# Kernel optimization log

Measured on AMD Instinct MI355X. Metric: run time of the kernel, lower is better.

Reference implementation:

```python
import jax, jax.numpy as jnp
import numpy as np

N, E = 100000, 1600000
IN, EDGE_DIM, HID, OUT, HEADS = 128, 16, 32, 32, 2


def _glorot(key, shape, scale=0.1):
    return jax.random.normal(key, shape, dtype=jnp.float32) * scale


def setup_inputs() -> dict:
    key = jax.random.key(0)
    ks = jax.random.split(key, 20)
    HC1 = HEADS * HID
    return {
        "x": jax.random.normal(ks[0], (N, IN), dtype=jnp.float32),
        "edge_index": jax.random.randint(ks[1], (2, E), 0, N, dtype=jnp.int32),
        "edge_attr": jax.random.normal(ks[2], (E, EDGE_DIM), dtype=jnp.float32),
        # layer 1 (heads=HEADS, concat=True)
        "W1l": _glorot(ks[3], (IN, HC1)), "b1l": jnp.zeros((HC1,), jnp.float32),
        "W1r": _glorot(ks[4], (IN, HC1)), "b1r": jnp.zeros((HC1,), jnp.float32),
        "W1e": _glorot(ks[5], (EDGE_DIM, HC1)),
        "att1": _glorot(ks[6], (HEADS, HID)),
        "bias1": jnp.zeros((HC1,), jnp.float32),
        # layer 2 (heads=1, concat=False)
        "W2l": _glorot(ks[7], (HC1, HID)), "b2l": jnp.zeros((HID,), jnp.float32),
        "W2r": _glorot(ks[8], (HC1, HID)), "b2r": jnp.zeros((HID,), jnp.float32),
        "W2e": _glorot(ks[9], (EDGE_DIM, HID)),
        "att2": _glorot(ks[10], (1, HID)),
        "bias2": jnp.zeros((HID,), jnp.float32),
        # final linear
        "Wlin": _glorot(ks[11], (HID, OUT)), "blin": jnp.zeros((OUT,), jnp.float32),
    }


def gatv2_layer(x, src, dst, edge_attr, Wl, bl, Wr, br, We, att, bias, H, C, concat):
    n = x.shape[0]
    xl = (x @ Wl + bl).reshape(n, H, C)   # source transform (lin_l)
    xr = (x @ Wr + br).reshape(n, H, C)   # target transform (lin_r)
    ea = (edge_attr @ We).reshape(-1, H, C)
    m = xl[src] + xr[dst] + ea                       # [E, H, C]
    e = jnp.sum(jax.nn.leaky_relu(m, 0.2) * att, axis=-1)  # [E, H]
    # segment softmax over incoming edges of each destination node
    emax = jax.ops.segment_max(e, dst, num_segments=n)
    emax = jnp.where(jnp.isfinite(emax), emax, 0.0)
    ee = jnp.exp(e - emax[dst])
    denom = jax.ops.segment_sum(ee, dst, num_segments=n)
    alpha = ee / (denom[dst] + 1e-16)                # [E, H]
    out = jax.ops.segment_sum(xl[src] * alpha[..., None], dst, num_segments=n)  # [N, H, C]
    out = out.reshape(n, H * C) if concat else out.mean(axis=1)
    return out + bias


def reference(x, edge_index, edge_attr, W1l, b1l, W1r, b1r, W1e, att1, bias1,
              W2l, b2l, W2r, b2r, W2e, att2, bias2, Wlin, blin):
    src, dst = edge_index[0], edge_index[1]
    h = jax.nn.elu(gatv2_layer(x, src, dst, edge_attr, W1l, b1l, W1r, b1r, W1e,
                               att1, bias1, HEADS, HID, True))
    h = jax.nn.elu(gatv2_layer(h, src, dst, edge_attr, W2l, b2l, W2r, b2r, W2e,
                               att2, bias2, 1, HID, False))
    return h @ Wlin + blin
```

## Files before the change

kernel.cpp:

```cpp
#include <hip/hip_runtime.h>
#include <hip/hip_fp16.h>
#include <cstdint>
#include <cstddef>


typedef _Float16 half8 __attribute__((ext_vector_type(8)));
typedef float f32x4 __attribute__((ext_vector_type(4)));

__global__ void hist_kernel(const int* __restrict__ dst, int* __restrict__ deg, int E) {
    int e = blockIdx.x * blockDim.x + threadIdx.x;
    if (e < E) atomicAdd(&deg[dst[e]], 1);
}

__global__ void scan_part(const int* __restrict__ deg, int* __restrict__ bsum, int n) {
    int tid = threadIdx.x;
    int base = blockIdx.x * 1024 + tid * 4;
    int s = 0;
#pragma unroll
    for (int j = 0; j < 4; ++j) {
        int i = base + j;
        if (i < n) s += deg[i];
    }
#pragma unroll
    for (int off = 1; off < 64; off <<= 1) s += __shfl_xor(s, off, 64);
    __shared__ int ws[4];
    if ((tid & 63) == 0) ws[tid >> 6] = s;
    __syncthreads();
    if (tid == 0) bsum[blockIdx.x] = ws[0] + ws[1] + ws[2] + ws[3];
}

__global__ void scan_mid(int* __restrict__ bsum, int* __restrict__ rowstart, int nb, int n) {
    int tid = threadIdx.x;
    int v = (tid < nb) ? bsum[tid] : 0;
    int incl = v;
#pragma unroll
    for (int off = 1; off < 64; off <<= 1) {
        int t = __shfl_up(incl, off, 64);
        if ((tid & 63) >= off) incl += t;
    }
    __shared__ int w0;
    if (tid == 63) w0 = incl;
    __syncthreads();
    if (tid >= 64) incl += w0;
    if (tid < nb) bsum[tid] = incl - v;
    if (tid == nb - 1) rowstart[n] = incl;
}

__global__ void scan_fin(const int* __restrict__ deg, const int* __restrict__ bsum,
                         int* __restrict__ rowstart, int n) {
    int tid = threadIdx.x;
    int lane = tid & 63, wid = tid >> 6;
    int base = blockIdx.x * 1024 + tid * 4;
    int v[4];
    int s = 0;
#pragma unroll
    for (int j = 0; j < 4; ++j) {
        int i = base + j;
        v[j] = (i < n) ? deg[i] : 0;
        s += v[j];
    }
    int incl = s;
#pragma unroll
    for (int off = 1; off < 64; off <<= 1) {
        int t = __shfl_up(incl, off, 64);
        if (lane >= off) incl += t;
    }
    __shared__ int ws[4];
    if (lane == 63) ws[wid] = incl;
    __syncthreads();
    int wofs = 0;
    for (int w2 = 0; w2 < wid; ++w2) wofs += ws[w2];
    int acc = bsum[blockIdx.x] + wofs + (incl - s);
#pragma unroll
    for (int j = 0; j < 4; ++j) {
        int i = base + j;
        if (i < n) rowstart[i] = acc;
        acc += v[j];
    }
}

__global__ void scatter_kernel(const int* __restrict__ src, const int* __restrict__ dst,
                               const float* __restrict__ eattr,
                               const int* __restrict__ rowstart, int* __restrict__ cursor,
                               int2* __restrict__ es, __half* __restrict__ eah, int E) {
    int e = blockIdx.x * blockDim.x + threadIdx.x;
    if (e < E) {
        int d = dst[e];
        int p = atomicAdd(&cursor[d], 1);
        es[rowstart[d] + p] = make_int2(e, src[e]);
        const float4* s4 = (const float4*)&eattr[(size_t)e * 16];
        float4 a = s4[0], b = s4[1], c = s4[2], f = s4[3];
        __half2 h[8];
        h[0] = __float22half2_rn(make_float2(a.x, a.y));
        h[1] = __float22half2_rn(make_float2(a.z, a.w));
        h[2] = __float22half2_rn(make_float2(b.x, b.y));
        h[3] = __float22half2_rn(make_float2(b.z, b.w));
        h[4] = __float22half2_rn(make_float2(c.x, c.y));
        h[5] = __float22half2_rn(make_float2(c.z, c.w));
        h[6] = __float22half2_rn(make_float2(f.x, f.y));
        h[7] = __float22half2_rn(make_float2(f.z, f.w));
        int4* o = (int4*)&eah[(size_t)e * 16];
        o[0] = *(int4*)&h[0];
        o[1] = *(int4*)&h[4];
    }
}

__global__ __launch_bounds__(1024) void dcount_block(const int* __restrict__ deg,
                                                     int* __restrict__ counts, int n) {
    __shared__ int h[256];
    int tid = threadIdx.x;
    if (tid < 256) h[tid] = 0;
    __syncthreads();
    int base = blockIdx.x * 4096 + tid;
#pragma unroll
    for (int j = 0; j < 4; ++j) {
        int i = base + j * 1024;
        if (i < n) {
            int b = deg[i];
            b = (b > 255) ? 255 : b;
            atomicAdd(&h[b], 1);
        }
    }
    __syncthreads();
    if (tid < 256) counts[blockIdx.x * 256 + tid] = h[tid];
}

__global__ void dbase_kernel(const int* __restrict__ counts, int* __restrict__ base, int nblk) {
    int b = threadIdx.x;
    int tot = 0;
    for (int k = 0; k < nblk; ++k) tot += counts[k * 256 + b];
    __shared__ int ws[4];
    int lane = b & 63, wid = b >> 6;
    int incl = tot;
#pragma unroll
    for (int off = 1; off < 64; off <<= 1) {
        int t = __shfl_up(incl, off, 64);
        if (lane >= off) incl += t;
    }
    if (lane == 63) ws[wid] = incl;
    __syncthreads();
    int wofs = 0;
    for (int w = 0; w < wid; ++w) wofs += ws[w];
    int acc = wofs + incl - tot;
    for (int k = 0; k < nblk; ++k) {
        base[k * 256 + b] = acc;
        acc += counts[k * 256 + b];
    }
}

__global__ __launch_bounds__(1024) void dscatter_block(const int* __restrict__ deg,
                                                       const int* __restrict__ base,
                                                       int* __restrict__ nodeperm, int n) {
    __shared__ int h[256];
    int tid = threadIdx.x;
    if (tid < 256) h[tid] = 0;
    __syncthreads();
    int bbase = blockIdx.x * 4096 + tid;
#pragma unroll
    for (int j = 0; j < 4; ++j) {
        int i = bbase + j * 1024;
        if (i < n) {
            int b = deg[i];
            b = (b > 255) ? 255 : b;
            int r = atomicAdd(&h[b], 1);
            nodeperm[base[blockIdx.x * 256 + b] + r] = i;
        }
    }
}

template <int K, int Mh>
__global__ void wprep_kernel(const float* __restrict__ Wl, const float* __restrict__ Wr,
                             __half* __restrict__ Wfrag) {
    constexpr int KS = K / 32;
    constexpr int BN = 2 * Mh;
    int i = blockIdx.x * blockDim.x + threadIdx.x;
    if (i >= K * BN) return;
    int j = i & 7;
    int lane = (i >> 3) & 63;
    int rest = i >> 9;
    int ks = rest % KS;
    int nt = rest / KS;
    int k = ks * 32 + ((lane >> 4) & 3) * 8 + j;
    int col = nt * 16 + (lane & 15);
    float v = (col < Mh) ? Wl[k * Mh + col] : Wr[k * Mh + (col - Mh)];
    Wfrag[i] = __float2half(v);
}

template <int K, int Mh, int BM>
__global__ __launch_bounds__(256) void gemm_mfma(
    const float* __restrict__ x, const __half* __restrict__ Wfrag,
    const float* __restrict__ bl, const float* __restrict__ br,
    __half* __restrict__ yl, __half* __restrict__ yr, int n) {
    constexpr int BN = 2 * Mh;
    constexpr int KS = K / 32;
    constexpr int NT = BN / 16;
    constexpr int RW = BM / 64;
    constexpr int LDP = K + 8;
    __shared__ __half xs[BM * LDP];
    int tid = threadIdx.x;
    int lane = tid & 63;
    int wave = tid >> 6;
    int node0 = blockIdx.x * BM;
    constexpr int ITER = (BM * K) / (256 * 4);
#pragma unroll
    for (int it = 0; it < ITER; ++it) {
        int base = (it * 256 + tid) * 4;
        int row = base / K, kk = base % K;
        float4 v = make_float4(0.f, 0.f, 0.f, 0.f);
        if (node0 + row < n) v = *(const float4*)&x[(size_t)(node0 + row) * K + kk];
        __half2* d = (__half2*)&xs[row * LDP + kk];
        d[0] = __float22half2_rn(make_float2(v.x, v.y));
        d[1] = __float22half2_rn(make_float2(v.z, v.w));
    }
    __syncthreads();
    f32x4 acc[RW][NT];
#pragma unroll
    for (int r = 0; r < RW; ++r)
#pragma unroll
        for (int t = 0; t < NT; ++t) {
            f32x4 z = {0.f, 0.f, 0.f, 0.f};
            acc[r][t] = z;
        }
    int r0 = lane & 15, kof = (lane >> 4) * 8;
#pragma unroll
    for (int ks = 0; ks < KS; ++ks) {
        half8 a[RW];
#pragma unroll
        for (int r = 0; r < RW; ++r) {
            int row = (wave * RW + r) * 16 + r0;
            a[r] = *reinterpret_cast<const half8*>(&xs[row * LDP + ks * 32 + kof]);
        }
#pragma unroll
        for (int t = 0; t < NT; ++t) {
            half8 b = *reinterpret_cast<const half8*>(&Wfrag[(((size_t)t * KS + ks) * 64 + lane) * 8]);
#pragma unroll
            for (int r = 0; r < RW; ++r)
                acc[r][t] = __builtin_amdgcn_mfma_f32_16x16x32_f16(a[r], b, acc[r][t], 0, 0, 0);
        }
    }
#pragma unroll
    for (int r = 0; r < RW; ++r) {
#pragma unroll
        for (int t = 0; t < NT; ++t) {
            int col = t * 16 + (lane & 15);
            float bv = (col < Mh) ? bl[col] : br[col - Mh];
#pragma unroll
            for (int q = 0; q < 4; ++q) {
                int node = node0 + (wave * RW + r) * 16 + (lane >> 4) * 4 + q;
                if (node < n) {
                    float v = acc[r][t][q] + bv;
                    if (col < Mh) yl[(size_t)node * Mh + col] = __float2half(v);
                    else          yr[(size_t)node * Mh + (col - Mh)] = __float2half(v);
                }
            }
        }
    }
}

template <int K, int M, int NPB>
__global__ void linear_kernel(const float* __restrict__ x, const float* __restrict__ W,
                              const float* __restrict__ b, float* __restrict__ y, int n) {
    __shared__ float sx[NPB * K];
    int tid = threadIdx.x;
    int node0 = blockIdx.x * NPB;
    for (int i = tid; i < NPB * K; i += NPB * M) {
        int nn = node0 + i / K;
        sx[i] = (nn < n) ? x[(size_t)nn * K + (i % K)] : 0.f;
    }
    __syncthreads();
    int ln = tid / M, m = tid % M;
    int node = node0 + ln;
    if (node >= n) return;
    float acc = b[m];
#pragma unroll
    for (int k = 0; k < K; ++k) acc = fmaf(sx[ln * K + k], W[k * M + m], acc);
    y[(size_t)node * M + m] = acc;
}

template <int H, int C>
__global__ __launch_bounds__(256) void fused_edge_agg(
    const int* __restrict__ rowstart, const int2* __restrict__ es,
    const __half* __restrict__ eah, const int* __restrict__ nodeperm,
    const float* __restrict__ We,
    const float* __restrict__ att,
    const __half* __restrict__ xl, const __half* __restrict__ xr,
    const float* __restrict__ bias, float* __restrict__ out, int n) {
    constexpr int HC = H * C;
    constexpr int LPN = HC / 2;
    constexpr int NPW = 64 / LPN;
    int gt = blockIdx.x * blockDim.x + threadIdx.x;
    int wave = gt >> 6;
    int lane = threadIdx.x & 63;
    int sub = lane / LPN;
    int j = lane % LPN;
    int ch0 = 2 * j;
    int slot = wave * NPW + sub;
    if (slot >= n) return;
    int node = nodeperm[slot];
    __half2 wh[16];
#pragma unroll
    for (int k = 0; k < 16; ++k) wh[k] = __float22half2_rn(*(const float2*)&We[k * HC + ch0]);
    float2 a2 = *(const float2*)&att[ch0];
    float2 xr2 = __half22float2(*(const __half2*)&xr[(size_t)node * HC + ch0]);
    int beg = rowstart[node], end = rowstart[node + 1];
    float denom = 0.f, acc0 = 0.f, acc1 = 0.f;

    auto gemv = [&](const float4& r0, const float4& r1, const __half2& xlh,
                    float& m0, float& m1, float2& xlf) {
        const __half2* h0 = (const __half2*)&r0;
        const __half2* h1 = (const __half2*)&r1;
        __half2 p0 = __hmul2(__low2half2(h0[0]), wh[0]);
        __half2 p1 = __hmul2(__high2half2(h0[0]), wh[1]);
        p0 = __hfma2(__low2half2(h0[1]), wh[2], p0);
        p1 = __hfma2(__high2half2(h0[1]), wh[3], p1);
        p0 = __hfma2(__low2half2(h0[2]), wh[4], p0);
        p1 = __hfma2(__high2half2(h0[2]), wh[5], p1);
        p0 = __hfma2(__low2half2(h0[3]), wh[6], p0);
        p1 = __hfma2(__high2half2(h0[3]), wh[7], p1);
        p0 = __hfma2(__low2half2(h1[0]), wh[8], p0);
        p1 = __hfma2(__high2half2(h1[0]), wh[9], p1);
        p0 = __hfma2(__low2half2(h1[1]), wh[10], p0);
        p1 = __hfma2(__high2half2(h1[1]), wh[11], p1);
        p0 = __hfma2(__low2half2(h1[2]), wh[12], p0);
        p1 = __hfma2(__high2half2(h1[2]), wh[13], p1);
        p0 = __hfma2(__low2half2(h1[3]), wh[14], p0);
        p1 = __hfma2(__high2half2(h1[3]), wh[15], p1);
        float2 mf = __half22float2(__hadd2(p0, p1));
        xlf = __half22float2(xlh);
        m0 = xlf.x + xr2.x + mf.x;
        m1 = xlf.y + xr2.y + mf.y;
    };
    auto logit = [&](float m0, float m1) -> float {
        m0 = (m0 > 0.f) ? m0 : 0.2f * m0;
        m1 = (m1 > 0.f) ? m1 : 0.2f * m1;
        float v = m0 * a2.x + m1 * a2.y;
#pragma unroll
        for (int msk = 1; msk < 16; msk <<= 1) v += __shfl_xor(v, msk, 64);
        return v;
    };

    int pp = beg;
    for (; pp + 2 <= end; pp += 2) {
        int2 ea = es[pp];
        int2 eb = es[pp + 1];
        const float4* qa = (const float4*)&eah[(size_t)ea.x * 16];
        const float4* qb = (const float4*)&eah[(size_t)eb.x * 16];
        float4 r0a = qa[0], r1a = qa[1];
        float4 r0b = qb[0], r1b = qb[1];
        __half2 xh0 = *(const __half2*)&xl[(size_t)ea.y * HC + ch0];
        __half2 xh1 = *(const __half2*)&xl[(size_t)eb.y * HC + ch0];
        float m0a, m1a, m0b, m1b;
        float2 xla, xlb;
        gemv(r0a, r1a, xh0, m0a, m1a, xla);
        gemv(r0b, r1b, xh1, m0b, m1b, xlb);
        float wa = __expf(logit(m0a, m1a));
        float wb = __expf(logit(m0b, m1b));
        denom += wa + wb;
        acc0 = fmaf(xla.x, wa, acc0);
        acc1 = fmaf(xla.y, wa, acc1);
        acc0 = fmaf(xlb.x, wb, acc0);
        acc1 = fmaf(xlb.y, wb, acc1);
    }
    if (pp < end) {
        int2 ea = es[pp];
        const float4* qa = (const float4*)&eah[(size_t)ea.x * 16];
        float4 r0a = qa[0], r1a = qa[1];
        __half2 xh0 = *(const __half2*)&xl[(size_t)ea.y * HC + ch0];
        float m0a, m1a;
        float2 xla;
        gemv(r0a, r1a, xh0, m0a, m1a, xla);
        float wa = __expf(logit(m0a, m1a));
        denom += wa;
        acc0 = fmaf(xla.x, wa, acc0);
        acc1 = fmaf(xla.y, wa, acc1);
    }
    float2 b2 = *(const float2*)&bias[ch0];
    float inv = 1.f / (denom + 1e-16f);
    float o0 = acc0 * inv + b2.x;
    float o1 = acc1 * inv + b2.y;
    o0 = (o0 > 0.f) ? o0 : __expf(o0) - 1.f;
    o1 = (o1 > 0.f) ? o1 : __expf(o1) - 1.f;
    *(float2*)&out[(size_t)node * HC + ch0] = make_float2(o0, o1);
}

extern "C" void kernel_launch(void* const* d_in, const int* in_sizes, int n_in,
                              void* d_out, int out_size, void* d_ws, size_t ws_size,
                              hipStream_t stream) {
    const float* x     = (const float*)d_in[0];
    const int*   eidx  = (const int*)d_in[1];
    const float* eattr = (const float*)d_in[2];
    const float* W1l   = (const float*)d_in[3];
    const float* b1l   = (const float*)d_in[4];
    const float* W1r   = (const float*)d_in[5];
    const float* b1r   = (const float*)d_in[6];
    const float* W1e   = (const float*)d_in[7];
    const float* att1  = (const float*)d_in[8];
    const float* bias1 = (const float*)d_in[9];
    const float* W2l   = (const float*)d_in[10];
    const float* b2l   = (const float*)d_in[11];
    const float* W2r   = (const float*)d_in[12];
    const float* b2r   = (const float*)d_in[13];
    const float* W2e   = (const float*)d_in[14];
    const float* att2  = (const float*)d_in[15];
    const float* bias2 = (const float*)d_in[16];
    const float* Wlin  = (const float*)d_in[17];
    const float* blin  = (const float*)d_in[18];

    const int N = in_sizes[0] / 128;
    const int E = in_sizes[1] / 2;
    const int* src = eidx;
    const int* dst = eidx + E;
    const int NBLK = (N + 4095) / 4096;

    char* p = (char*)d_ws;
    auto take = [&](size_t bytes) {
        char* r = p;
        p += (bytes + 255) & ~(size_t)255;
        return r;
    };
    int*    deg      = (int*)take((size_t)N * sizeof(int));
    int*    cursor   = (int*)take((size_t)N * sizeof(int));
    char*   zero_end = p;
    int*    rowstart = (int*)take((size_t)(N + 1) * sizeof(int));
    int*    bsum     = (int*)take(256 * sizeof(int));
    int*    counts   = (int*)take((size_t)(NBLK + 1) * 256 * sizeof(int));
    int*    dbase    = (int*)take((size_t)(NBLK + 1) * 256 * sizeof(int));
    int*    nodeperm = (int*)take((size_t)N * sizeof(int));
    int2*   es       = (int2*)take((size_t)E * sizeof(int2));
    __half* eah      = (__half*)take((size_t)E * 16 * sizeof(__half));
    __half* A        = (__half*)take((size_t)N * 64 * sizeof(__half));
    __half* B        = (__half*)take((size_t)N * 64 * sizeof(__half));
    float*  Cbuf     = (float*)take((size_t)N * 64 * sizeof(float));
    __half* Wf1      = (__half*)take((size_t)128 * 128 * sizeof(__half));
    __half* Wf2      = (__half*)take((size_t)64 * 64 * sizeof(__half));

    (void)hipMemsetAsync(deg, 0, (size_t)(zero_end - (char*)deg), stream);
    hist_kernel<<<(E + 255) / 256, 256, 0, stream>>>(dst, deg, E);
    {
        int nb = (N + 1023) / 1024;
        scan_part<<<nb, 256, 0, stream>>>(deg, bsum, N);
        scan_mid<<<1, 128, 0, stream>>>(bsum, rowstart, nb, N);
        scan_fin<<<nb, 256, 0, stream>>>(deg, bsum, rowstart, N);
    }
    scatter_kernel<<<(E + 255) / 256, 256, 0, stream>>>(src, dst, eattr, rowstart, cursor, es,
                                                        eah, E);
    dcount_block<<<NBLK, 1024, 0, stream>>>(deg, counts, N);
    dbase_kernel<<<1, 256, 0, stream>>>(counts, dbase, NBLK);
    dscatter_block<<<NBLK, 1024, 0, stream>>>(deg, dbase, nodeperm, N);
    wprep_kernel<128, 64><<<(128 * 128 + 255) / 256, 256, 0, stream>>>(W1l, W1r, Wf1);
    wprep_kernel<64, 32><<<(64 * 64 + 255) / 256, 256, 0, stream>>>(W2l, W2r, Wf2);

    gemm_mfma<128, 64, 64><<<(N + 63) / 64, 256, 0, stream>>>(x, Wf1, b1l, b1r, A, B, N);
    {
        long waves = (N + 1) / 2;
        fused_edge_agg<2, 32><<<(int)((waves * 64 + 255) / 256), 256, 0, stream>>>(
            rowstart, es, eah, nodeperm, W1e, att1, A, B, bias1, Cbuf, N);
    }

    gemm_mfma<64, 32, 128><<<(N + 127) / 128, 256, 0, stream>>>(Cbuf, Wf2, b2l, b2r, A, B, N);
    {
        long waves = (N + 3) / 4;
        fused_edge_agg<1, 32><<<(int)((waves * 64 + 255) / 256), 256, 0, stream>>>(
            rowstart, es, eah, nodeperm, W2e, att2, A, B, bias2, Cbuf, N);
    }

    linear_kernel<32, 32, 8><<<(N + 7) / 8, 256, 0, stream>>>(Cbuf, Wlin, blin, (float*)d_out, N);
}
```

Measured before the change: 421.2 us.

## Fuse setup kernels into one launch and materialize dst-sorted edge attributes

Merges the layer-1 GEMM, the edge scatter and the degree-count kernels into a single multi-role launch, and merges the two weight-prep kernels into one. The interleaved (eid,src) array is split into separate eid and src arrays. When workspace allows, layer-1 edge aggregation writes the edge attributes in destination-sorted order so layer 2 reads them contiguously instead of gathering by edge id. This trades an extra write of the edge-attribute buffer and more workspace for fewer launches and a coalesced read in layer 2.

```diff
diff --git a/kernel.cpp b/kernel.cpp
--- a/kernel.cpp
+++ b/kernel.cpp
@@ -79,15 +79,109 @@
     }
 }
 
-__global__ void scatter_kernel(const int* __restrict__ src, const int* __restrict__ dst,
-                               const float* __restrict__ eattr,
-                               const int* __restrict__ rowstart, int* __restrict__ cursor,
-                               int2* __restrict__ es, __half* __restrict__ eah, int E) {
-    int e = blockIdx.x * blockDim.x + threadIdx.x;
+template <int K, int Mh>
+__device__ void wprep_body(int i, const float* __restrict__ Wl, const float* __restrict__ Wr,
+                           __half* __restrict__ Wfrag) {
+    constexpr int KS = K / 32;
+    if (i >= K * 2 * Mh) return;
+    int j = i & 7;
+    int lane = (i >> 3) & 63;
+    int rest = i >> 9;
+    int ks = rest % KS;
+    int nt = rest / KS;
+    int k = ks * 32 + ((lane >> 4) & 3) * 8 + j;
+    int col = nt * 16 + (lane & 15);
+    float v = (col < Mh) ? Wl[k * Mh + col] : Wr[k * Mh + (col - Mh)];
+    Wfrag[i] = __float2half(v);
+}
+
+__global__ void wprep_both(const float* W1l, const float* W1r, __half* Wf1,
+                           const float* W2l, const float* W2r, __half* Wf2) {
+    int bid = blockIdx.x;
+    int tid = threadIdx.x;
+    if (bid < 64) wprep_body<128, 64>(bid * 256 + tid, W1l, W1r, Wf1);
+    else          wprep_body<64, 32>((bid - 64) * 256 + tid, W2l, W2r, Wf2);
+}
+
+template <int K, int Mh, int BM>
+__device__ void gemm_body(int bid, __half* xs, const float* __restrict__ x,
+                          const __half* __restrict__ Wfrag, const float* __restrict__ bl,
+                          const float* __restrict__ br, __half* __restrict__ yl,
+                          __half* __restrict__ yr, int n) {
+    constexpr int KS = K / 32;
+    constexpr int NT = (2 * Mh) / 16;
+    constexpr int RW = BM / 64;
+    constexpr int LDP = K + 8;
+    int tid = threadIdx.x;
+    int lane = tid & 63;
+    int wave = tid >> 6;
+    int node0 = bid * BM;
+    constexpr int ITER = (BM * K) / (256 * 4);
+#pragma unroll
+    for (int it = 0; it < ITER; ++it) {
+        int base = (it * 256 + tid) * 4;
+        int row = base / K, kk = base % K;
+        float4 v = make_float4(0.f, 0.f, 0.f, 0.f);
+        if (node0 + row < n) v = *(const float4*)&x[(size_t)(node0 + row) * K + kk];
+        __half2* d = (__half2*)&xs[row * LDP + kk];
+        d[0] = __float22half2_rn(make_float2(v.x, v.y));
+        d[1] = __float22half2_rn(make_float2(v.z, v.w));
+    }
+    __syncthreads();
+    f32x4 acc[RW][NT];
+#pragma unroll
+    for (int r = 0; r < RW; ++r)
+#pragma unroll
+        for (int t = 0; t < NT; ++t) {
+            f32x4 z = {0.f, 0.f, 0.f, 0.f};
+            acc[r][t] = z;
+        }
+    int r0 = lane & 15, kof = (lane >> 4) * 8;
+#pragma unroll
+    for (int ks = 0; ks < KS; ++ks) {
+        half8 a[RW];
+#pragma unroll
+        for (int r = 0; r < RW; ++r) {
+            int row = (wave * RW + r) * 16 + r0;
+            a[r] = *reinterpret_cast<const half8*>(&xs[row * LDP + ks * 32 + kof]);
+        }
+#pragma unroll
+        for (int t = 0; t < NT; ++t) {
+            half8 b = *reinterpret_cast<const half8*>(&Wfrag[(((size_t)t * KS + ks) * 64 + lane) * 8]);
+#pragma unroll
+            for (int r = 0; r < RW; ++r)
+                acc[r][t] = __builtin_amdgcn_mfma_f32_16x16x32_f16(a[r], b, acc[r][t], 0, 0, 0);
+        }
+    }
+#pragma unroll
+    for (int r = 0; r < RW; ++r) {
+#pragma unroll
+        for (int t = 0; t < NT; ++t) {
+            int col = t * 16 + (lane & 15);
+            float bv = (col < Mh) ? bl[col] : br[col - Mh];
+#pragma unroll
+            for (int q = 0; q < 4; ++q) {
+                int node = node0 + (wave * RW + r) * 16 + (lane >> 4) * 4 + q;
+                if (node < n) {
+                    float v = acc[r][t][q] + bv;
+                    if (col < Mh) yl[(size_t)node * Mh + col] = __float2half(v);
+                    else          yr[(size_t)node * Mh + (col - Mh)] = __float2half(v);
+                }
+            }
+        }
+    }
+}
+
+__device__ void scatter_body(int e, const int* __restrict__ src, const int* __restrict__ dst,
+                             const float* __restrict__ eattr, const int* __restrict__ rowstart,
+                             int* __restrict__ cursor, int* __restrict__ eid_sorted,
+                             int* __restrict__ src_sorted, __half* __restrict__ eah, int E) {
     if (e < E) {
         int d = dst[e];
         int p = atomicAdd(&cursor[d], 1);
-        es[rowstart[d] + p] = make_int2(e, src[e]);
+        int pos = rowstart[d] + p;
+        eid_sorted[pos] = e;
+        src_sorted[pos] = src[e];
         const float4* s4 = (const float4*)&eattr[(size_t)e * 16];
         float4 a = s4[0], b = s4[1], c = s4[2], f = s4[3];
         __half2 h[8];
@@ -105,16 +199,15 @@
     }
 }
 
-__global__ __launch_bounds__(1024) void dcount_block(const int* __restrict__ deg,
-                                                     int* __restrict__ counts, int n) {
-    __shared__ int h[256];
-    int tid = threadIdx.x;
-    if (tid < 256) h[tid] = 0;
-    __syncthreads();
-    int base = blockIdx.x * 4096 + tid;
-#pragma unroll
-    for (int j = 0; j < 4; ++j) {
-        int i = base + j * 1024;
+__device__ void dcount_body(int bid, int* h, const int* __restrict__ deg,
+                            int* __restrict__ counts, int n) {
+    int tid = threadIdx.x;
+    h[tid] = 0;
+    __syncthreads();
+    int base = bid * 4096;
+#pragma unroll
+    for (int j = 0; j < 16; ++j) {
+        int i = base + j * 256 + tid;
         if (i < n) {
             int b = deg[i];
             b = (b > 255) ? 255 : b;
@@ -122,7 +215,30 @@
         }
     }
     __syncthreads();
-    if (tid < 256) counts[blockIdx.x * 256 + tid] = h[tid];
+    counts[bid * 256 + tid] = h[tid];
+}
+
+__global__ __launch_bounds__(256) void fat_kernel(
+    int nbG, int nbS,
+    const float* __restrict__ x, const __half* __restrict__ Wf1,
+    const float* __restrict__ b1l, const float* __restrict__ b1r,
+    __half* __restrict__ A, __half* __restrict__ B, int n,
+    const int* __restrict__ src, const int* __restrict__ dst,
+    const float* __restrict__ eattr, const int* __restrict__ rowstart,
+    int* __restrict__ cursor, int* __restrict__ eid_sorted, int* __restrict__ src_sorted,
+    __half* __restrict__ eah, int E,
+    const int* __restrict__ deg, int* __restrict__ counts) {
+    __shared__ __half xs[64 * 136];
+    __shared__ int hcnt[256];
+    int bid = blockIdx.x;
+    if (bid < nbG) {
+        gemm_body<128, 64, 64>(bid, xs, x, Wf1, b1l, b1r, A, B, n);
+    } else if (bid < nbG + nbS) {
+        scatter_body((bid - nbG) * 256 + threadIdx.x, src, dst, eattr, rowstart, cursor,
+                     eid_sorted, src_sorted, eah, E);
+    } else {
+        dcount_body(bid - nbG - nbS, hcnt, deg, counts, n);
+    }
 }
 
 __global__ void dbase_kernel(const int* __restrict__ counts, int* __restrict__ base, int nblk) {
@@ -148,17 +264,17 @@
     }
 }
 
-__global__ __launch_bounds__(1024) void dscatter_block(const int* __restrict__ deg,
-                                                       const int* __restrict__ base,
-                                                       int* __restrict__ nodeperm, int n) {
+__global__ __launch_bounds__(256) void dscatter_block(const int* __restrict__ deg,
+                                                      const int* __restrict__ base,
+                                                      int* __restrict__ nodeperm, int n) {
     __shared__ int h[256];
     int tid = threadIdx.x;
-    if (tid < 256) h[tid] = 0;
-    __syncthreads();
-    int bbase = blockIdx.x * 4096 + tid;
-#pragma unroll
-    for (int j = 0; j < 4; ++j) {
-        int i = bbase + j * 1024;
+    h[tid] = 0;
+    __syncthreads();
+    int bbase = blockIdx.x * 4096;
+#pragma unroll
+    for (int j = 0; j < 16; ++j) {
+        int i = bbase + j * 256 + tid;
         if (i < n) {
             int b = deg[i];
             b = (b > 255) ? 255 : b;
@@ -168,93 +284,13 @@
     }
 }
 
-template <int K, int Mh>
-__global__ void wprep_kernel(const float* __restrict__ Wl, const float* __restrict__ Wr,
-                             __half* __restrict__ Wfrag) {
-    constexpr int KS = K / 32;
-    constexpr int BN = 2 * Mh;
-    int i = blockIdx.x * blockDim.x + threadIdx.x;
-    if (i >= K * BN) return;
-    int j = i & 7;
-    int lane = (i >> 3) & 63;
-    int rest = i >> 9;
-    int ks = rest % KS;
-    int nt = rest / KS;
-    int k = ks * 32 + ((lane >> 4) & 3) * 8 + j;
-    int col = nt * 16 + (lane & 15);
-    float v = (col < Mh) ? Wl[k * Mh + col] : Wr[k * Mh + (col - Mh)];
-    Wfrag[i] = __float2half(v);
-}
-
 template <int K, int Mh, int BM>
 __global__ __launch_bounds__(256) void gemm_mfma(
     const float* __restrict__ x, const __half* __restrict__ Wfrag,
     const float* __restrict__ bl, const float* __restrict__ br,
     __half* __restrict__ yl, __half* __restrict__ yr, int n) {
-    constexpr int BN = 2 * Mh;
-    constexpr int KS = K / 32;
-    constexpr int NT = BN / 16;
-    constexpr int RW = BM / 64;
-    constexpr int LDP = K + 8;
-    __shared__ __half xs[BM * LDP];
-    int tid = threadIdx.x;
-    int lane = tid & 63;
-    int wave = tid >> 6;
-    int node0 = blockIdx.x * BM;
-    constexpr int ITER = (BM * K) / (256 * 4);
-#pragma unroll
-    for (int it = 0; it < ITER; ++it) {
-        int base = (it * 256 + tid) * 4;
-        int row = base / K, kk = base % K;
-        float4 v = make_float4(0.f, 0.f, 0.f, 0.f);
-        if (node0 + row < n) v = *(const float4*)&x[(size_t)(node0 + row) * K + kk];
-        __half2* d = (__half2*)&xs[row * LDP + kk];
-        d[0] = __float22half2_rn(make_float2(v.x, v.y));
-        d[1] = __float22half2_rn(make_float2(v.z, v.w));
-    }
-    __syncthreads();
-    f32x4 acc[RW][NT];
-#pragma unroll
-    for (int r = 0; r < RW; ++r)
-#pragma unroll
-        for (int t = 0; t < NT; ++t) {
-            f32x4 z = {0.f, 0.f, 0.f, 0.f};
-            acc[r][t] = z;
-        }
-    int r0 = lane & 15, kof = (lane >> 4) * 8;
-#pragma unroll
-    for (int ks = 0; ks < KS; ++ks) {
-        half8 a[RW];
-#pragma unroll
-        for (int r = 0; r < RW; ++r) {
-            int row = (wave * RW + r) * 16 + r0;
-            a[r] = *reinterpret_cast<const half8*>(&xs[row * LDP + ks * 32 + kof]);
-        }
-#pragma unroll
-        for (int t = 0; t < NT; ++t) {
-            half8 b = *reinterpret_cast<const half8*>(&Wfrag[(((size_t)t * KS + ks) * 64 + lane) * 8]);
-#pragma unroll
-            for (int r = 0; r < RW; ++r)
-                acc[r][t] = __builtin_amdgcn_mfma_f32_16x16x32_f16(a[r], b, acc[r][t], 0, 0, 0);
-        }
-    }
-#pragma unroll
-    for (int r = 0; r < RW; ++r) {
-#pragma unroll
-        for (int t = 0; t < NT; ++t) {
-            int col = t * 16 + (lane & 15);
-            float bv = (col < Mh) ? bl[col] : br[col - Mh];
-#pragma unroll
-            for (int q = 0; q < 4; ++q) {
-                int node = node0 + (wave * RW + r) * 16 + (lane >> 4) * 4 + q;
-                if (node < n) {
-                    float v = acc[r][t][q] + bv;
-                    if (col < Mh) yl[(size_t)node * Mh + col] = __float2half(v);
-                    else          yr[(size_t)node * Mh + (col - Mh)] = __float2half(v);
-                }
-            }
-        }
-    }
+    __shared__ __half xs[BM * (K + 8)];
+    gemm_body<K, Mh, BM>(blockIdx.x, xs, x, Wfrag, bl, br, yl, yr, n);
 }
 
 template <int K, int M, int NPB>
@@ -277,10 +313,11 @@
     y[(size_t)node * M + m] = acc;
 }
 
-template <int H, int C>
+template <int H, int C, int MODE>
 __global__ __launch_bounds__(256) void fused_edge_agg(
-    const int* __restrict__ rowstart, const int2* __restrict__ es,
-    const __half* __restrict__ eah, const int* __restrict__ nodeperm,
+    const int* __restrict__ rowstart, const int* __restrict__ eid_sorted,
+    const int* __restrict__ src_sorted, const __half* __restrict__ eah,
+    __half* __restrict__ eah_sorted, const int* __restrict__ nodeperm,
     const float* __restrict__ We,
     const float* __restrict__ att,
     const __half* __restrict__ xl, const __half* __restrict__ xr,
@@ -305,6 +342,18 @@
     int beg = rowstart[node], end = rowstart[node + 1];
     float denom = 0.f, acc0 = 0.f, acc1 = 0.f;
 
+    auto load_rows = [&](int pp, float4& r0, float4& r1) {
+        if (MODE == 1) {
+            const float4* q = (const float4*)&eah_sorted[(size_t)pp * 16];
+            r0 = q[0];
+            r1 = q[1];
+        } else {
+            int eid = eid_sorted[pp];
+            const float4* q = (const float4*)&eah[(size_t)eid * 16];
+            r0 = q[0];
+            r1 = q[1];
+        }
+    };
     auto gemv = [&](const float4& r0, const float4& r1, const __half2& xlh,
                     float& m0, float& m1, float2& xlf) {
         const __half2* h0 = (const __half2*)&r0;
@@ -341,14 +390,18 @@
 
     int pp = beg;
     for (; pp + 2 <= end; pp += 2) {
-        int2 ea = es[pp];
-        int2 eb = es[pp + 1];
-        const float4* qa = (const float4*)&eah[(size_t)ea.x * 16];
-        const float4* qb = (const float4*)&eah[(size_t)eb.x * 16];
-        float4 r0a = qa[0], r1a = qa[1];
-        float4 r0b = qb[0], r1b = qb[1];
-        __half2 xh0 = *(const __half2*)&xl[(size_t)ea.y * HC + ch0];
-        __half2 xh1 = *(const __half2*)&xl[(size_t)eb.y * HC + ch0];
+        float4 r0a, r1a, r0b, r1b;
+        load_rows(pp, r0a, r1a);
+        load_rows(pp + 1, r0b, r1b);
+        __half2 xh0 = *(const __half2*)&xl[(size_t)src_sorted[pp] * HC + ch0];
+        __half2 xh1 = *(const __half2*)&xl[(size_t)src_sorted[pp + 1] * HC + ch0];
+        if (MODE == 0 && j == 0) {
+            float4* o = (float4*)&eah_sorted[(size_t)pp * 16];
+            o[0] = r0a;
+            o[1] = r1a;
+            o[2] = r0b;
+            o[3] = r1b;
+        }
         float m0a, m1a, m0b, m1b;
         float2 xla, xlb;
         gemv(r0a, r1a, xh0, m0a, m1a, xla);
@@ -362,10 +415,14 @@
         acc1 = fmaf(xlb.y, wb, acc1);
     }
     if (pp < end) {
-        int2 ea = es[pp];
-        const float4* qa = (const float4*)&eah[(size_t)ea.x * 16];
-        float4 r0a = qa[0], r1a = qa[1];
-        __half2 xh0 = *(const __half2*)&xl[(size_t)ea.y * HC + ch0];
+        float4 r0a, r1a;
+        load_rows(pp, r0a, r1a);
+        __half2 xh0 = *(const __half2*)&xl[(size_t)src_sorted[pp] * HC + ch0];
+        if (MODE == 0 && j == 0) {
+            float4* o = (float4*)&eah_sorted[(size_t)pp * 16];
+            o[0] = r0a;
+            o[1] = r1a;
+        }
         float m0a, m1a;
         float2 xla;
         gemv(r0a, r1a, xh0, m0a, m1a, xla);
@@ -410,7 +467,7 @@
     const int E = in_sizes[1] / 2;
     const int* src = eidx;
     const int* dst = eidx + E;
-    const int NBLK = (N + 4095) / 4096;
+    const int NB_DC = (N + 4095) / 4096;
 
     char* p = (char*)d_ws;
     auto take = [&](size_t bytes) {
@@ -418,21 +475,26 @@
         p += (bytes + 255) & ~(size_t)255;
         return r;
     };
-    int*    deg      = (int*)take((size_t)N * sizeof(int));
-    int*    cursor   = (int*)take((size_t)N * sizeof(int));
-    char*   zero_end = p;
-    int*    rowstart = (int*)take((size_t)(N + 1) * sizeof(int));
-    int*    bsum     = (int*)take(256 * sizeof(int));
-    int*    counts   = (int*)take((size_t)(NBLK + 1) * 256 * sizeof(int));
-    int*    dbase    = (int*)take((size_t)(NBLK + 1) * 256 * sizeof(int));
-    int*    nodeperm = (int*)take((size_t)N * sizeof(int));
-    int2*   es       = (int2*)take((size_t)E * sizeof(int2));
-    __half* eah      = (__half*)take((size_t)E * 16 * sizeof(__half));
-    __half* A        = (__half*)take((size_t)N * 64 * sizeof(__half));
-    __half* B        = (__half*)take((size_t)N * 64 * sizeof(__half));
-    float*  Cbuf     = (float*)take((size_t)N * 64 * sizeof(float));
-    __half* Wf1      = (__half*)take((size_t)128 * 128 * sizeof(__half));
-    __half* Wf2      = (__half*)take((size_t)64 * 64 * sizeof(__half));
+    int*    deg        = (int*)take((size_t)N * sizeof(int));
+    int*    cursor     = (int*)take((size_t)N * sizeof(int));
+    char*   zero_end   = p;
+    int*    rowstart   = (int*)take((size_t)(N + 1) * sizeof(int));
+    int*    bsum       = (int*)take(256 * sizeof(int));
+    int*    counts     = (int*)take((size_t)(NB_DC + 1) * 256 * sizeof(int));
+    int*    dbase      = (int*)take((size_t)(NB_DC + 1) * 256 * sizeof(int));
+    int*    nodeperm   = (int*)take((size_t)N * sizeof(int));
+    int*    eid_sorted = (int*)take((size_t)E * sizeof(int));
+    int*    src_sorted = (int*)take((size_t)E * sizeof(int));
+    __half* eah        = (__half*)take((size_t)E * 16 * sizeof(__half));
+    __half* A          = (__half*)take((size_t)N * 64 * sizeof(__half));
+    __half* B          = (__half*)take((size_t)N * 64 * sizeof(__half));
+    float*  Cbuf       = (float*)take((size_t)N * 64 * sizeof(float));
+    __half* Wf1        = (__half*)take((size_t)128 * 128 * sizeof(__half));
+    __half* Wf2        = (__half*)take((size_t)64 * 64 * sizeof(__half));
+    size_t used = (size_t)(p - (char*)d_ws);
+    size_t ea_bytes = (size_t)E * 16 * sizeof(__half);
+    int have_ws = (ws_size >= used + ea_bytes + 512) ? 1 : 0;
+    __half* eah_sorted = have_ws ? (__half*)take(ea_bytes) : (__half*)nullptr;
 
     (void)hipMemsetAsync(deg, 0, (size_t)(zero_end - (char*)deg), stream);
     hist_kernel<<<(E + 255) / 256, 256, 0, stream>>>(dst, deg, E);
@@ -442,26 +504,43 @@
         scan_mid<<<1, 128, 0, stream>>>(bsum, rowstart, nb, N);
         scan_fin<<<nb, 256, 0, stream>>>(deg, bsum, rowstart, N);
     }
-    scatter_kernel<<<(E + 255) / 256, 256, 0, stream>>>(src, dst, eattr, rowstart, cursor, es,
-                                                        eah, E);
-    dcount_block<<<NBLK, 1024, 0, stream>>>(deg, counts, N);
-    dbase_kernel<<<1, 256, 0, stream>>>(counts, dbase, NBLK);
-    dscatter_block<<<NBLK, 1024, 0, stream>>>(deg, dbase, nodeperm, N);
-    wprep_kernel<128, 64><<<(128 * 128 + 255) / 256, 256, 0, stream>>>(W1l, W1r, Wf1);
-    wprep_kernel<64, 32><<<(64 * 64 + 255) / 256, 256, 0, stream>>>(W2l, W2r, Wf2);
-
-    gemm_mfma<128, 64, 64><<<(N + 63) / 64, 256, 0, stream>>>(x, Wf1, b1l, b1r, A, B, N);
+    wprep_both<<<80, 256, 0, stream>>>(W1l, W1r, Wf1, W2l, W2r, Wf2);
+
+    {
+        int nbG = (N + 63) / 64;
+        int nbS = (E + 255) / 256;
+        fat_kernel<<<nbG + nbS + NB_DC, 256, 0, stream>>>(
+            nbG, nbS, x, Wf1, b1l, b1r, A, B, N, src, dst, eattr, rowstart, cursor, eid_sorted,
+            src_sorted, eah, E, deg, counts);
+    }
+    dbase_kernel<<<1, 256, 0, stream>>>(counts, dbase, NB_DC);
+    dscatter_block<<<NB_DC, 256, 0, stream>>>(deg, dbase, nodeperm, N);
+
     {
         long waves = (N + 1) / 2;
-        fused_edge_agg<2, 32><<<(int)((waves * 64 + 255) / 256), 256, 0, stream>>>(
-            rowstart, es, eah, nodeperm, W1e, att1, A, B, bias1, Cbuf, N);
+        int grid = (int)((waves * 64 + 255) / 256);
+        if (have_ws)
+            fused_edge_agg<2, 32, 0><<<grid, 256, 0, stream>>>(
+                rowstart, eid_sorted, src_sorted, eah, eah_sorted, nodeperm, W1e, att1, A, B,
+                bias1, Cbuf, N);
+        else
+            fused_edge_agg<2, 32, 2><<<grid, 256, 0, stream>>>(
+                rowstart, eid_sorted, src_sorted, eah, nullptr, nodeperm, W1e, att1, A, B,
+                bias1, Cbuf, N);
     }
 
     gemm_mfma<64, 32, 128><<<(N + 127) / 128, 256, 0, stream>>>(Cbuf, Wf2, b2l, b2r, A, B, N);
     {
         long waves = (N + 3) / 4;
-        fused_edge_agg<1, 32><<<(int)((waves * 64 + 255) / 256), 256, 0, stream>>>(
-            rowstart, es, eah, nodeperm, W2e, att2, A, B, bias2, Cbuf, N);
+        int grid = (int)((waves * 64 + 255) / 256);
+        if (have_ws)
+            fused_edge_agg<1, 32, 1><<<grid, 256, 0, stream>>>(
+                rowstart, eid_sorted, src_sorted, eah, eah_sorted, nodeperm, W2e, att2, A, B,
+                bias2, Cbuf, N);
+        else
+            fused_edge_agg<1, 32, 2><<<grid, 256, 0, stream>>>(
+                rowstart, eid_sorted, src_sorted, eah, nullptr, nodeperm, W2e, att2, A, B,
+                bias2, Cbuf, N);
     }
 
     linear_kernel<32, 32, 8><<<(N + 7) / 8, 256, 0, stream>>>(Cbuf, Wlin, blin, (float*)d_out, N);
```

Result: slower. 482.2 us (+14.5%).

## Merge independent preprocessing kernels into one heterogeneous launch

Applied to the files above, without the earlier changes.

Combines the layer-1 GEMM, the edge scatter and the degree-count histogram into a single kernel that dispatches on block index, and merges the two weight-prep kernels into one launch. It also shrinks the degree-bucketing kernels from 1024 to 256 threads per block, with 16 iterations each. The aim is to cut launch count and let independent work overlap on the GPU instead of running serially. In exchange, every block of the fused kernel reserves the GEMM's shared memory, which may lower occupancy for the scatter and histogram blocks.

```diff
diff --git a/kernel.cpp b/kernel.cpp
--- a/kernel.cpp
+++ b/kernel.cpp
@@ -79,11 +79,103 @@
     }
 }
 
-__global__ void scatter_kernel(const int* __restrict__ src, const int* __restrict__ dst,
-                               const float* __restrict__ eattr,
-                               const int* __restrict__ rowstart, int* __restrict__ cursor,
-                               int2* __restrict__ es, __half* __restrict__ eah, int E) {
-    int e = blockIdx.x * blockDim.x + threadIdx.x;
+template <int K, int Mh>
+__device__ void wprep_body(int i, const float* __restrict__ Wl, const float* __restrict__ Wr,
+                           __half* __restrict__ Wfrag) {
+    constexpr int KS = K / 32;
+    if (i >= K * 2 * Mh) return;
+    int j = i & 7;
+    int lane = (i >> 3) & 63;
+    int rest = i >> 9;
+    int ks = rest % KS;
+    int nt = rest / KS;
+    int k = ks * 32 + ((lane >> 4) & 3) * 8 + j;
+    int col = nt * 16 + (lane & 15);
+    float v = (col < Mh) ? Wl[k * Mh + col] : Wr[k * Mh + (col - Mh)];
+    Wfrag[i] = __float2half(v);
+}
+
+__global__ void wprep_both(const float* W1l, const float* W1r, __half* Wf1,
+                           const float* W2l, const float* W2r, __half* Wf2) {
+    int bid = blockIdx.x;
+    int tid = threadIdx.x;
+    if (bid < 64) wprep_body<128, 64>(bid * 256 + tid, W1l, W1r, Wf1);
+    else          wprep_body<64, 32>((bid - 64) * 256 + tid, W2l, W2r, Wf2);
+}
+
+template <int K, int Mh, int BM>
+__device__ void gemm_body(int bid, __half* xs, const float* __restrict__ x,
+                          const __half* __restrict__ Wfrag, const float* __restrict__ bl,
+                          const float* __restrict__ br, __half* __restrict__ yl,
+                          __half* __restrict__ yr, int n) {
+    constexpr int KS = K / 32;
+    constexpr int NT = (2 * Mh) / 16;
+    constexpr int RW = BM / 64;
+    constexpr int LDP = K + 8;
+    int tid = threadIdx.x;
+    int lane = tid & 63;
+    int wave = tid >> 6;
+    int node0 = bid * BM;
+    constexpr int ITER = (BM * K) / (256 * 4);
+#pragma unroll
+    for (int it = 0; it < ITER; ++it) {
+        int base = (it * 256 + tid) * 4;
+        int row = base / K, kk = base % K;
+        float4 v = make_float4(0.f, 0.f, 0.f, 0.f);
+        if (node0 + row < n) v = *(const float4*)&x[(size_t)(node0 + row) * K + kk];
+        __half2* d = (__half2*)&xs[row * LDP + kk];
+        d[0] = __float22half2_rn(make_float2(v.x, v.y));
+        d[1] = __float22half2_rn(make_float2(v.z, v.w));
+    }
+    __syncthreads();
+    f32x4 acc[RW][NT];
+#pragma unroll
+    for (int r = 0; r < RW; ++r)
+#pragma unroll
+        for (int t = 0; t < NT; ++t) {
+            f32x4 z = {0.f, 0.f, 0.f, 0.f};
+            acc[r][t] = z;
+        }
+    int r0 = lane & 15, kof = (lane >> 4) * 8;
+#pragma unroll
+    for (int ks = 0; ks < KS; ++ks) {
+        half8 a[RW];
+#pragma unroll
+        for (int r = 0; r < RW; ++r) {
+            int row = (wave * RW + r) * 16 + r0;
+            a[r] = *reinterpret_cast<const half8*>(&xs[row * LDP + ks * 32 + kof]);
+        }
+#pragma unroll
+        for (int t = 0; t < NT; ++t) {
+            half8 b = *reinterpret_cast<const half8*>(&Wfrag[(((size_t)t * KS + ks) * 64 + lane) * 8]);
+#pragma unroll
+            for (int r = 0; r < RW; ++r)
+                acc[r][t] = __builtin_amdgcn_mfma_f32_16x16x32_f16(a[r], b, acc[r][t], 0, 0, 0);
+        }
+    }
+#pragma unroll
+    for (int r = 0; r < RW; ++r) {
+#pragma unroll
+        for (int t = 0; t < NT; ++t) {
+            int col = t * 16 + (lane & 15);
+            float bv = (col < Mh) ? bl[col] : br[col - Mh];
+#pragma unroll
+            for (int q = 0; q < 4; ++q) {
+                int node = node0 + (wave * RW + r) * 16 + (lane >> 4) * 4 + q;
+                if (node < n) {
+                    float v = acc[r][t][q] + bv;
+                    if (col < Mh) yl[(size_t)node * Mh + col] = __float2half(v);
+                    else          yr[(size_t)node * Mh + (col - Mh)] = __float2half(v);
+                }
+            }
+        }
+    }
+}
+
+__device__ void scatter_body(int e, const int* __restrict__ src, const int* __restrict__ dst,
+                             const float* __restrict__ eattr, const int* __restrict__ rowstart,
+                             int* __restrict__ cursor, int2* __restrict__ es,
+                             __half* __restrict__ eah, int E) {
     if (e < E) {
         int d = dst[e];
         int p = atomicAdd(&cursor[d], 1);
@@ -105,16 +197,15 @@
     }
 }
 
-__global__ __launch_bounds__(1024) void dcount_block(const int* __restrict__ deg,
-                                                     int* __restrict__ counts, int n) {
-    __shared__ int h[256];
-    int tid = threadIdx.x;
-    if (tid < 256) h[tid] = 0;
-    __syncthreads();
-    int base = blockIdx.x * 4096 + tid;
-#pragma unroll
-    for (int j = 0; j < 4; ++j) {
-        int i = base + j * 1024;
+__device__ void dcount_body(int bid, int* h, const int* __restrict__ deg,
+                            int* __restrict__ counts, int n) {
+    int tid = threadIdx.x;
+    h[tid] = 0;
+    __syncthreads();
+    int base = bid * 4096;
+#pragma unroll
+    for (int j = 0; j < 16; ++j) {
+        int i = base + j * 256 + tid;
         if (i < n) {
             int b = deg[i];
             b = (b > 255) ? 255 : b;
@@ -122,7 +213,29 @@
         }
     }
     __syncthreads();
-    if (tid < 256) counts[blockIdx.x * 256 + tid] = h[tid];
+    counts[bid * 256 + tid] = h[tid];
+}
+
+__global__ __launch_bounds__(256) void fat_kernel(
+    int nbG, int nbS,
+    const float* __restrict__ x, const __half* __restrict__ Wf1,
+    const float* __restrict__ b1l, const float* __restrict__ b1r,
+    __half* __restrict__ A, __half* __restrict__ B, int n,
+    const int* __restrict__ src, const int* __restrict__ dst,
+    const float* __restrict__ eattr, const int* __restrict__ rowstart,
+    int* __restrict__ cursor, int2* __restrict__ es, __half* __restrict__ eah, int E,
+    const int* __restrict__ deg, int* __restrict__ counts) {
+    __shared__ __half xs[64 * 136];
+    __shared__ int hcnt[256];
+    int bid = blockIdx.x;
+    if (bid < nbG) {
+        gemm_body<128, 64, 64>(bid, xs, x, Wf1, b1l, b1r, A, B, n);
+    } else if (bid < nbG + nbS) {
+        scatter_body((bid - nbG) * 256 + threadIdx.x, src, dst, eattr, rowstart, cursor, es,
+                     eah, E);
+    } else {
+        dcount_body(bid - nbG - nbS, hcnt, deg, counts, n);
+    }
 }
 
 __global__ void dbase_kernel(const int* __restrict__ counts, int* __restrict__ base, int nblk) {
@@ -148,17 +261,17 @@
     }
 }
 
-__global__ __launch_bounds__(1024) void dscatter_block(const int* __restrict__ deg,
-                                                       const int* __restrict__ base,
-                                                       int* __restrict__ nodeperm, int n) {
+__global__ __launch_bounds__(256) void dscatter_block(const int* __restrict__ deg,
+                                                      const int* __restrict__ base,
+                                                      int* __restrict__ nodeperm, int n) {
     __shared__ int h[256];
     int tid = threadIdx.x;
-    if (tid < 256) h[tid] = 0;
-    __syncthreads();
-    int bbase = blockIdx.x * 4096 + tid;
-#pragma unroll
-    for (int j = 0; j < 4; ++j) {
-        int i = bbase + j * 1024;
+    h[tid] = 0;
+    __syncthreads();
+    int bbase = blockIdx.x * 4096;
+#pragma unroll
+    for (int j = 0; j < 16; ++j) {
+        int i = bbase + j * 256 + tid;
         if (i < n) {
             int b = deg[i];
             b = (b > 255) ? 255 : b;
@@ -168,93 +281,13 @@
     }
 }
 
-template <int K, int Mh>
-__global__ void wprep_kernel(const float* __restrict__ Wl, const float* __restrict__ Wr,
-                             __half* __restrict__ Wfrag) {
-    constexpr int KS = K / 32;
-    constexpr int BN = 2 * Mh;
-    int i = blockIdx.x * blockDim.x + threadIdx.x;
-    if (i >= K * BN) return;
-    int j = i & 7;
-    int lane = (i >> 3) & 63;
-    int rest = i >> 9;
-    int ks = rest % KS;
-    int nt = rest / KS;
-    int k = ks * 32 + ((lane >> 4) & 3) * 8 + j;
-    int col = nt * 16 + (lane & 15);
-    float v = (col < Mh) ? Wl[k * Mh + col] : Wr[k * Mh + (col - Mh)];
-    Wfrag[i] = __float2half(v);
-}
-
 template <int K, int Mh, int BM>
 __global__ __launch_bounds__(256) void gemm_mfma(
     const float* __restrict__ x, const __half* __restrict__ Wfrag,
     const float* __restrict__ bl, const float* __restrict__ br,
     __half* __restrict__ yl, __half* __restrict__ yr, int n) {
-    constexpr int BN = 2 * Mh;
-    constexpr int KS = K / 32;
-    constexpr int NT = BN / 16;
-    constexpr int RW = BM / 64;
-    constexpr int LDP = K + 8;
-    __shared__ __half xs[BM * LDP];
-    int tid = threadIdx.x;
-    int lane = tid & 63;
-    int wave = tid >> 6;
-    int node0 = blockIdx.x * BM;
-    constexpr int ITER = (BM * K) / (256 * 4);
-#pragma unroll
-    for (int it = 0; it < ITER; ++it) {
-        int base = (it * 256 + tid) * 4;
-        int row = base / K, kk = base % K;
-        float4 v = make_float4(0.f, 0.f, 0.f, 0.f);
-        if (node0 + row < n) v = *(const float4*)&x[(size_t)(node0 + row) * K + kk];
-        __half2* d = (__half2*)&xs[row * LDP + kk];
-        d[0] = __float22half2_rn(make_float2(v.x, v.y));
-        d[1] = __float22half2_rn(make_float2(v.z, v.w));
-    }
-    __syncthreads();
-    f32x4 acc[RW][NT];
-#pragma unroll
-    for (int r = 0; r < RW; ++r)
-#pragma unroll
-        for (int t = 0; t < NT; ++t) {
-            f32x4 z = {0.f, 0.f, 0.f, 0.f};
-            acc[r][t] = z;
-        }
-    int r0 = lane & 15, kof = (lane >> 4) * 8;
-#pragma unroll
-    for (int ks = 0; ks < KS; ++ks) {
-        half8 a[RW];
-#pragma unroll
-        for (int r = 0; r < RW; ++r) {
-            int row = (wave * RW + r) * 16 + r0;
-            a[r] = *reinterpret_cast<const half8*>(&xs[row * LDP + ks * 32 + kof]);
-        }
-#pragma unroll
-        for (int t = 0; t < NT; ++t) {
-            half8 b = *reinterpret_cast<const half8*>(&Wfrag[(((size_t)t * KS + ks) * 64 + lane) * 8]);
-#pragma unroll
-            for (int r = 0; r < RW; ++r)
-                acc[r][t] = __builtin_amdgcn_mfma_f32_16x16x32_f16(a[r], b, acc[r][t], 0, 0, 0);
-        }
-    }
-#pragma unroll
-    for (int r = 0; r < RW; ++r) {
-#pragma unroll
-        for (int t = 0; t < NT; ++t) {
-            int col = t * 16 + (lane & 15);
-            float bv = (col < Mh) ? bl[col] : br[col - Mh];
-#pragma unroll
-            for (int q = 0; q < 4; ++q) {
-                int node = node0 + (wave * RW + r) * 16 + (lane >> 4) * 4 + q;
-                if (node < n) {
-                    float v = acc[r][t][q] + bv;
-                    if (col < Mh) yl[(size_t)node * Mh + col] = __float2half(v);
-                    else          yr[(size_t)node * Mh + (col - Mh)] = __float2half(v);
-                }
-            }
-        }
-    }
+    __shared__ __half xs[BM * (K + 8)];
+    gemm_body<K, Mh, BM>(blockIdx.x, xs, x, Wfrag, bl, br, yl, yr, n);
 }
 
 template <int K, int M, int NPB>
@@ -410,7 +443,7 @@
     const int E = in_sizes[1] / 2;
     const int* src = eidx;
     const int* dst = eidx + E;
-    const int NBLK = (N + 4095) / 4096;
+    const int NB_DC = (N + 4095) / 4096;
 
     char* p = (char*)d_ws;
     auto take = [&](size_t bytes) {
@@ -423,8 +456,8 @@
     char*   zero_end = p;
     int*    rowstart = (int*)take((size_t)(N + 1) * sizeof(int));
     int*    bsum     = (int*)take(256 * sizeof(int));
-    int*    counts   = (int*)take((size_t)(NBLK + 1) * 256 * sizeof(int));
-    int*    dbase    = (int*)take((size_t)(NBLK + 1) * 256 * sizeof(int));
+    int*    counts   = (int*)take((size_t)(NB_DC + 1) * 256 * sizeof(int));
+    int*    dbase    = (int*)take((size_t)(NB_DC + 1) * 256 * sizeof(int));
     int*    nodeperm = (int*)take((size_t)N * sizeof(int));
     int2*   es       = (int2*)take((size_t)E * sizeof(int2));
     __half* eah      = (__half*)take((size_t)E * 16 * sizeof(__half));
@@ -442,15 +475,18 @@
         scan_mid<<<1, 128, 0, stream>>>(bsum, rowstart, nb, N);
         scan_fin<<<nb, 256, 0, stream>>>(deg, bsum, rowstart, N);
     }
-    scatter_kernel<<<(E + 255) / 256, 256, 0, stream>>>(src, dst, eattr, rowstart, cursor, es,
-                                                        eah, E);
-    dcount_block<<<NBLK, 1024, 0, stream>>>(deg, counts, N);
-    dbase_kernel<<<1, 256, 0, stream>>>(counts, dbase, NBLK);
-    dscatter_block<<<NBLK, 1024, 0, stream>>>(deg, dbase, nodeperm, N);
-    wprep_kernel<128, 64><<<(128 * 128 + 255) / 256, 256, 0, stream>>>(W1l, W1r, Wf1);
-    wprep_kernel<64, 32><<<(64 * 64 + 255) / 256, 256, 0, stream>>>(W2l, W2r, Wf2);
-
-    gemm_mfma<128, 64, 64><<<(N + 63) / 64, 256, 0, stream>>>(x, Wf1, b1l, b1r, A, B, N);
+    wprep_both<<<80, 256, 0, stream>>>(W1l, W1r, Wf1, W2l, W2r, Wf2);
+
+    {
+        int nbG = (N + 63) / 64;
+        int nbS = (E + 255) / 256;
+        fat_kernel<<<nbG + nbS + NB_DC, 256, 0, stream>>>(
+            nbG, nbS, x, Wf1, b1l, b1r, A, B, N, src, dst, eattr, rowstart, cursor, es, eah, E,
+            deg, counts);
+    }
+    dbase_kernel<<<1, 256, 0, stream>>>(counts, dbase, NB_DC);
+    dscatter_block<<<NB_DC, 256, 0, stream>>>(deg, dbase, nodeperm, N);
+
     {
         long waves = (N + 1) / 2;
         fused_edge_agg<2, 32><<<(int)((waves * 64 + 255) / 256), 256, 0, stream>>>(
```

After: 408.0 us. 1.03x faster.
